# Kernel tuning notes

Measured on AMD Instinct MI355X. Metric: run time of the kernel, lower is better.

Reference implementation:

```python
import jax, jax.numpy as jnp
import numpy as np

# ---- config (matches init_kwargs) ----
M, N, D = 8, 512, 243            # meshes, neurons per mesh, input dim
E_RATIO = 0.8
NE = int(N * E_RATIO)            # 409 excitatory
NI = N - NE                      # 103 inhibitory
TICKS = 16
BATCH = 512
BITS = 4
WSCALE = 8.0
VTH, VRESET = 1.0, 0.0
TAU_E, TAU_I, DT = 2.0, 1.5, 1.0
BETA = 10.0                      # fast-sigmoid surrogate slope
INPUT_SCALE = 1.0


def fake_quant(w):
    """Quantization-aware fake quant with straight-through estimator."""
    step = WSCALE / (2 ** (BITS - 1))          # 1.0 for 4-bit, scale 8
    q = jnp.clip(jnp.round(w / step), -(2 ** (BITS - 1)), 2 ** (BITS - 1) - 1) * step
    return w + jax.lax.stop_gradient(q - w)


@jax.custom_vjp
def spike(u):
    return (u >= 0.0).astype(u.dtype)

def _spike_fwd(u):
    return spike(u), u

def _spike_bwd(u, g):
    # fast-sigmoid surrogate gradient
    return (g * BETA / (1.0 + BETA * jnp.abs(u)) ** 2,)

spike.defvjp(_spike_fwd, _spike_bwd)


def setup_inputs() -> dict:
    key = jax.random.key(0)
    ks = jax.random.split(key, 8)

    def sparse_w(k, shape, density, std, zero_diag=False):
        km, kw = jax.random.split(k)
        mask = (jax.random.uniform(km, shape) < density).astype(jnp.float32)
        if zero_diag:
            mask = mask * (1.0 - jnp.eye(shape[-1], dtype=jnp.float32))
        return jax.random.normal(kw, shape) * std * mask

    x = jax.random.normal(ks[0], (BATCH, D), dtype=jnp.float32)
    W_in = jax.random.normal(ks[1], (M, N, D)) * 0.8      # per-mesh input projection [out,in]
    b_in = jax.random.normal(ks[2], (M, N)) * 0.05
    W_inter = sparse_w(ks[3], (M, N, NE), 0.3, 0.8)        # inter-mesh: E of mesh m -> mesh m+1
    W_EE = sparse_w(ks[4], (M, NE, NE), 0.5, 0.8, True)
    W_EI = sparse_w(ks[5], (M, NI, NE), 0.6, 0.8)
    W_IE = sparse_w(ks[6], (M, NE, NI), 0.8, 0.8)
    W_II = sparse_w(ks[7], (M, NI, NI), 0.7, 0.8, True)
    return dict(x=x, W_in=W_in, b_in=b_in, W_inter=W_inter,
                W_EE=W_EE, W_EI=W_EI, W_IE=W_IE, W_II=W_II)


def reference(x, W_in, b_in, W_inter, W_EE, W_EI, W_IE, W_II):
    B = x.shape[0]
    decay_E = 1.0 - DT / TAU_E
    decay_I = 1.0 - DT / TAU_I

    # quantize weights once (constant across ticks)
    qW_in, qW_inter = fake_quant(W_in), fake_quant(W_inter)
    qW_EE, qW_EI = fake_quant(W_EE), fake_quant(W_EI)
    qW_IE, qW_II = fake_quant(W_IE), fake_quant(W_II)

    # external input projection, same every tick: [M, B, N]
    ext_proj = jnp.einsum('bd,mnd->mbn', x * INPUT_SCALE, qW_in) + b_in[:, None, :]

    def tick(carry, _):
        e, i, vE, vI, acc = carry          # e:[M,B,NE] i:[M,B,NI]
        # inter-mesh: mesh m receives inter_connections[m-1](e_prev[m-1])
        inter = jnp.einsum('mbe,mne->mbn', e, qW_inter)
        ext = ext_proj + jnp.roll(inter, 1, axis=0)
        cE = ext[:, :, :NE] \
            + jnp.einsum('mbe,mfe->mbf', e, qW_EE) \
            + jnp.einsum('mbi,mfi->mbf', i, qW_IE)
        cI = ext[:, :, NE:] \
            + jnp.einsum('mbe,mfe->mbf', e, qW_EI) \
            + jnp.einsum('mbi,mfi->mbf', i, qW_II)
        # LIF: leaky decay + input, threshold, hard reset
        vE = vE * decay_E + cE * DT
        vI = vI * decay_I + cI * DT
        sE = spike(vE - VTH)
        sI = spike(vI - VTH)
        vE = sE * VRESET + (1.0 - sE) * vE
        vI = sI * VRESET + (1.0 - sI) * vI
        acc = acc + jnp.concatenate([sE, sI], axis=-1)
        return (sE, sI, vE, vI, acc), None

    z = jnp.zeros
    carry0 = (z((M, B, NE)), z((M, B, NI)), z((M, B, NE)), z((M, B, NI)), z((M, B, N)))
    (eF, iF, vEF, vIF, acc), _ = jax.lax.scan(tick, carry0, None, length=TICKS)
    # accumulator laid out mesh-major: [B, M*N]
    return jnp.transpose(acc, (1, 0, 2)).reshape(B, M * N)
```

## Files before the change

### kernel.cpp

```cpp
#include <hip/hip_runtime.h>
#include <hip/hip_bf16.h>

#define Mm 8
#define Nn 512
#define NEe 409
#define NIi 103
#define Bb 512
#define Dd 243
#define Tt 16
#define SPB 96
#define SPTICK (Mm * Bb * SPB)
#define WCROW 1152
#define DEC_I 0.33333334f
#define NBLK 256
#define FLAGSTRIDE 16
#define SPINMAX 1000000L
#define ABROW 176
#define ZSPAN_U32 1581056

typedef int v4i __attribute__((ext_vector_type(4)));

__device__ __forceinline__ float quantf(float w) {
    float q = rintf(w);
    return fminf(fmaxf(q, -8.0f), 7.0f);
}

__device__ __forceinline__ v4i unpack16(unsigned int dl, unsigned int dh, bool qhi, int qsh) {
    unsigned int d = qhi ? dh : dl;
    v4i r;
    r[0] = (int)((((d >> qsh) & 0xFu) * 0x00204081u) & 0x01010101u);
    r[1] = (int)((((d >> (qsh + 4)) & 0xFu) * 0x00204081u) & 0x01010101u);
    r[2] = (int)((((d >> (qsh + 8)) & 0xFu) * 0x00204081u) & 0x01010101u);
    r[3] = (int)((((d >> (qsh + 12)) & 0xFu) * 0x00204081u) & 0x01010101u);
    return r;
}

__global__ void k_pack(const float* __restrict__ Wint, const float* __restrict__ WEE,
                       const float* __restrict__ WEI, const float* __restrict__ WIE,
                       const float* __restrict__ WII, signed char* __restrict__ Wc,
                       unsigned* __restrict__ spz) {
    int gid = blockIdx.x * 256 + threadIdx.x;
#pragma unroll
    for (int z = 0; z < 2; ++z) {
        int i = gid + z * 1179648;
        if (i < ZSPAN_U32) spz[i] = 0u;
    }
    int q = gid;
    if (q >= (Mm * Nn * WCROW) / 4) return;
    int k0 = (q * 4) % WCROW;
    int n  = ((q * 4) / WCROW) & (Nn - 1);
    int m  = (q * 4) / (WCROW * Nn);
    char out4[4];
#pragma unroll
    for (int j = 0; j < 4; ++j) {
        int k = k0 + j;
        float w = 0.0f;
        if (k < 512) {
            if (k < NEe) w = Wint[((((m + 7) & 7) * Nn) + n) * NEe + k];
        } else if (k < 1024) {
            int jj = k - 512;
            if (jj < NEe) w = (n < NEe) ? WEE[((m * NEe) + n) * NEe + jj]
                                        : WEI[((m * NIi) + (n - NEe)) * NEe + jj];
        } else {
            int jj = k - 1049;
            if (jj >= 0 && jj < NIi) w = (n < NEe) ? WIE[((m * NEe) + n) * NIi + jj]
                                        : WII[((m * NIi) + (n - NEe)) * NIi + jj];
        }
        out4[j] = (signed char)(int)quantf(w);
    }
    *(int*)&Wc[q * 4] = *(int*)out4;
}

__global__ void __launch_bounds__(512, 2)
k_ticks(const signed char* __restrict__ Wc,
        unsigned char* __restrict__ Sp,
        const float* __restrict__ x,
        const float* __restrict__ Win,
        const float* __restrict__ bin,
        float* __restrict__ out,
        int* __restrict__ flags) {
    __shared__ __align__(16) signed char sB[128 * WCROW];
    __shared__ __align__(16) unsigned char sAb[64 * ABROW];

    const int wg = blockIdx.x;
    const int m  = wg & 7;
    const int bt = (wg >> 3) & 7;
    const int nt = wg >> 6;
    const int b0 = bt * 64;
    const int n0 = nt * 128;
    const int pm = (m + 7) & 7;

    const int tid  = threadIdx.x;
    const int w    = tid >> 6;
    const int lane = tid & 63;
    const int bh   = w & 1;
    const int nh   = w >> 1;
    const int quad = lane >> 4;
    const int li   = lane & 15;

    int waitIdx = 0;
    if (tid < 8) {
        int mm = (tid < 4) ? pm : m;
        waitIdx = (((tid & 3) << 6) | (bt << 3) | mm) * FLAGSTRIDE;
    }

    float decs[2]; int nels[2];
    int styp[2], soff[2];
#pragma unroll
    for (int tn = 0; tn < 2; ++tn) {
        int n = n0 + nh * 32 + tn * 16 + li;
        nels[tn] = n;
        decs[tn] = (n < NEe) ? 0.5f : DEC_I;
        int nb = n0 + nh * 32 + tn * 16;
        if (nb < 400)      { styp[tn] = 0; soff[tn] = nb >> 3; }
        else if (nb == 400){ styp[tn] = 2; soff[tn] = 50; }
        else               { styp[tn] = 1; soff[tn] = 64 + ((nb - 384) >> 3); }
    }
    const int bbase = b0 + bh * 32;

    {
        const int g   = tid >> 8;
        const int t8  = tid & 255;
        const int n0e = n0 + g * 64;
        float* xs  = (float*)sB + g * (2 * 64 * 68);
        float* wsm = xs + 64 * 68;
        const int etb4 = (t8 & 15) * 4;
        const int etn4 = (t8 >> 4) * 4;
        const int sr = t8 >> 2;
        const int sc = (t8 & 3) * 16;
        float c[4][4];
#pragma unroll
        for (int i = 0; i < 4; ++i)
#pragma unroll
            for (int j = 0; j < 4; ++j) c[i][j] = 0.0f;

        for (int d0 = 0; d0 < Dd; d0 += 64) {
#pragma unroll
            for (int j = 0; j < 16; ++j) {
                int d = d0 + sc + j;
                float xv = 0.0f, wv = 0.0f;
                if (d < Dd) {
                    xv = x[(b0 + sr) * Dd + d];
                    wv = quantf(Win[((m * Nn) + n0e + sr) * Dd + d]);
                }
                xs[(sc + j) * 68 + sr] = xv;
                wsm[(sc + j) * 68 + sr] = wv;
            }
            __syncthreads();
            const int dmax = min(64, Dd - d0);
            for (int d = 0; d < dmax; ++d) {
                float4 av = *(const float4*)&xs[d * 68 + etb4];
                float4 wv = *(const float4*)&wsm[d * 68 + etn4];
                float a[4] = {av.x, av.y, av.z, av.w};
                float wq[4] = {wv.x, wv.y, wv.z, wv.w};
#pragma unroll
                for (int i = 0; i < 4; ++i)
#pragma unroll
                    for (int j = 0; j < 4; ++j)
                        c[i][j] = fmaf(a[i], wq[j], c[i][j]);
            }
            __syncthreads();
        }
        float* extbuf = (float*)sB;
#pragma unroll
        for (int i = 0; i < 4; ++i)
#pragma unroll
            for (int j = 0; j < 4; ++j)
                extbuf[(etb4 + i) * 128 + g * 64 + etn4 + j] =
                    __fadd_rn(c[i][j], bin[m * Nn + n0e + etn4 + j]);
        __syncthreads();
    }

    float extr[2][2][4];
#pragma unroll
    for (int tb = 0; tb < 2; ++tb)
#pragma unroll
        for (int tn = 0; tn < 2; ++tn)
#pragma unroll
            for (int r = 0; r < 4; ++r)
                extr[tb][tn][r] = ((const float*)sB)[(bh * 32 + tb * 16 + quad * 4 + r) * 128
                                                     + (nels[tn] - n0)];
    __syncthreads();

    const signed char* WcBase = Wc + (size_t)(m * Nn + n0) * WCROW;
#pragma unroll
    for (int j = 0; j < 18; ++j) {
        int task = tid + j * 512;
        int row = task / 72, gg = task % 72;
        v4i v = *(const v4i*)(WcBase + (size_t)row * WCROW + gg * 16);
        int gs = (gg < 64) ? ((gg & 48) | ((gg ^ row) & 15))
                           : (64 + ((gg ^ row) & 7));
        *(v4i*)&sB[row * WCROW + gs * 16] = v;
    }
    if (tid < 384) {
        int row = tid / 6, z = tid - (tid / 6) * 6;
        int s = (z < 3) ? (13 + z) : (26 + z);
        *(unsigned*)&sAb[row * ABROW + s * 4] = 0u;
    }
    __syncthreads();

    float vmem[2][2][4];
    int cnt[2][2];
#pragma unroll
    for (int tb = 0; tb < 2; ++tb)
#pragma unroll
        for (int tn = 0; tn < 2; ++tn) {
            cnt[tb][tn] = 0;
#pragma unroll
            for (int r = 0; r < 4; ++r) vmem[tb][tn][r] = 0.0f;
        }

    const bool qhi = (quad >= 2);
    const int qsh = (quad & 1) << 4;
    const int r0base = (bh * 32 + li) * ABROW;
    const int r1base = (bh * 32 + 16 + li) * ABROW;

    for (int t = 0; t < Tt; ++t) {
        float c[2][2][4];

        if (t == 0) {
#pragma unroll
            for (int tb = 0; tb < 2; ++tb)
#pragma unroll
                for (int tn = 0; tn < 2; ++tn)
#pragma unroll
                    for (int r = 0; r < 4; ++r)
                        c[tb][tn][r] = __fadd_rn(__fadd_rn(__fadd_rn(extr[tb][tn][r], 0.0f), 0.0f), 0.0f);
        } else {
            if (tid < 8) {
                long spin = 0;
                while (__hip_atomic_load(&flags[waitIdx],
                                         __ATOMIC_RELAXED, __HIP_MEMORY_SCOPE_AGENT) < t) {
                    __builtin_amdgcn_s_sleep(2);
                    if (++spin > SPINMAX) break;
                }
            }
            __syncthreads();

            const unsigned char* SR = Sp + (size_t)(t - 1) * SPTICK;
            const unsigned char* PrevRow = SR + (size_t)(pm * Bb + b0) * SPB;
            const unsigned char* OwnRow  = SR + (size_t)(m  * Bb + b0) * SPB;
#pragma unroll
            for (int j = 0; j < 3; ++j) {
                int task = tid + j * 512;
                if (task < 1152) {
                    int row = task / 18, s = task % 18;
                    const unsigned char* src;
                    int dstoff;
                    if (s < 8)       { src = PrevRow + (size_t)row * SPB + s * 8;            dstoff = s * 8; }
                    else if (s < 16) { src = OwnRow  + (size_t)row * SPB + (s - 8) * 8;      dstoff = s * 8; }
                    else             { src = OwnRow  + (size_t)row * SPB + 64 + (s - 16) * 8; dstoff = 128 + (s - 16) * 8; }
                    unsigned long long vb = __hip_atomic_load((const unsigned long long*)src,
                                               __ATOMIC_RELAXED, __HIP_MEMORY_SCOPE_AGENT);
                    *(unsigned long long*)&sAb[row * ABROW + dstoff] = vb;
                }
            }
            __syncthreads();

            v4i acc[2][2];
#pragma unroll
            for (int tb = 0; tb < 2; ++tb)
#pragma unroll
                for (int tn = 0; tn < 2; ++tn) acc[tb][tn] = (v4i){0, 0, 0, 0};

#pragma unroll
            for (int ch = 0; ch < 4; ++ch) {
                const int cb = ch << 8;
                v4i a0lo = *(const v4i*)&sAb[r0base + (cb >> 3)];
                v4i a0hi = *(const v4i*)&sAb[r0base + (cb >> 3) + 16];
                v4i a1lo = *(const v4i*)&sAb[r1base + (cb >> 3)];
                v4i a1hi = *(const v4i*)&sAb[r1base + (cb >> 3) + 16];
#pragma unroll
                for (int ks = 0; ks < 256; ks += 64) {
                    v4i s0 = (ks < 128) ? a0lo : a0hi;
                    v4i s1 = (ks < 128) ? a1lo : a1hi;
                    const int D0 = ((ks >> 6) & 1) ? 2 : 0;
                    v4i af0 = unpack16((unsigned int)s0[D0], (unsigned int)s0[D0 + 1], qhi, qsh);
                    v4i af1 = unpack16((unsigned int)s1[D0], (unsigned int)s1[D0 + 1], qhi, qsh);
                    const int gs = (cb >> 4) + ((((ks >> 4) + quad) ^ li) & 15);
#pragma unroll
                    for (int tn = 0; tn < 2; ++tn) {
                        const v4i bfr = *(const v4i*)&sB[(nh * 32 + tn * 16 + li) * WCROW + gs * 16];
                        acc[0][tn] = __builtin_amdgcn_mfma_i32_16x16x64_i8(af0, bfr, acc[0][tn], 0, 0, 0);
                        acc[1][tn] = __builtin_amdgcn_mfma_i32_16x16x64_i8(af1, bfr, acc[1][tn], 0, 0, 0);
                    }
                }
                if (ch == 1) {
#pragma unroll
                    for (int tb = 0; tb < 2; ++tb)
#pragma unroll
                        for (int tn = 0; tn < 2; ++tn) {
#pragma unroll
                            for (int r = 0; r < 4; ++r)
                                c[tb][tn][r] = __fadd_rn(extr[tb][tn][r], (float)acc[tb][tn][r]);
                            acc[tb][tn] = (v4i){0, 0, 0, 0};
                        }
                } else if (ch == 3) {
#pragma unroll
                    for (int tb = 0; tb < 2; ++tb)
#pragma unroll
                        for (int tn = 0; tn < 2; ++tn) {
#pragma unroll
                            for (int r = 0; r < 4; ++r)
                                c[tb][tn][r] = __fadd_rn(c[tb][tn][r], (float)acc[tb][tn][r]);
                            acc[tb][tn] = (v4i){0, 0, 0, 0};
                        }
                }
            }
            {
                v4i e0 = *(const v4i*)&sAb[r0base + 128];
                v4i e1 = *(const v4i*)&sAb[r1base + 128];
#pragma unroll
                for (int ks = 0; ks < 128; ks += 64) {
                    const int D0 = (ks >> 6) ? 2 : 0;
                    v4i af0 = unpack16((unsigned int)e0[D0], (unsigned int)e0[D0 + 1], qhi, qsh);
                    v4i af1 = unpack16((unsigned int)e1[D0], (unsigned int)e1[D0 + 1], qhi, qsh);
                    const int gs = 64 + ((((ks >> 4) + quad) ^ li) & 7);
#pragma unroll
                    for (int tn = 0; tn < 2; ++tn) {
                        const v4i bfr = *(const v4i*)&sB[(nh * 32 + tn * 16 + li) * WCROW + gs * 16];
                        acc[0][tn] = __builtin_amdgcn_mfma_i32_16x16x64_i8(af0, bfr, acc[0][tn], 0, 0, 0);
                        acc[1][tn] = __builtin_amdgcn_mfma_i32_16x16x64_i8(af1, bfr, acc[1][tn], 0, 0, 0);
                    }
                }
            }
#pragma unroll
            for (int tb = 0; tb < 2; ++tb)
#pragma unroll
                for (int tn = 0; tn < 2; ++tn)
#pragma unroll
                    for (int r = 0; r < 4; ++r)
                        c[tb][tn][r] = __fadd_rn(c[tb][tn][r], (float)acc[tb][tn][r]);
        }

        int snow[2][2] = {{0, 0}, {0, 0}};
#pragma unroll
        for (int tb = 0; tb < 2; ++tb)
#pragma unroll
            for (int tn = 0; tn < 2; ++tn)
#pragma unroll
                for (int r = 0; r < 4; ++r) {
                    float vn = __fadd_rn(__fmul_rn(vmem[tb][tn][r], decs[tn]), c[tb][tn][r]);
                    int s = (vn >= 1.0f) ? 1 : 0;
                    vmem[tb][tn][r] = s ? 0.0f : vn;
                    cnt[tb][tn] += s << (r * 8);
                    snow[tb][tn] |= s << r;
                }

        if (t < Tt - 1) {
            unsigned char* SW = Sp + (size_t)t * SPTICK;
#pragma unroll
            for (int tb = 0; tb < 2; ++tb)
#pragma unroll
                for (int tn = 0; tn < 2; ++tn)
#pragma unroll
                    for (int r = 0; r < 4; ++r) {
                        unsigned long long mk = __ballot((snow[tb][tn] >> r) & 1);
                        if (li == 0) {
                            unsigned short v = (unsigned short)(mk >> (unsigned)(quad << 4));
                            int row = bbase + tb * 16 + quad * 4 + r;
                            unsigned char* rb = SW + (size_t)(m * Bb + row) * SPB;
                            if (styp[tn] != 2) {
                                __hip_atomic_store((unsigned short*)(rb + soff[tn]), v,
                                                   __ATOMIC_RELAXED, __HIP_MEMORY_SCOPE_AGENT);
                            } else {
                                __hip_atomic_store((unsigned short*)(rb + 50),
                                                   (unsigned short)(v & 0x01FF),
                                                   __ATOMIC_RELAXED, __HIP_MEMORY_SCOPE_AGENT);
                                __hip_atomic_store((unsigned short*)(rb + 66),
                                                   (unsigned short)(v & 0xFE00),
                                                   __ATOMIC_RELAXED, __HIP_MEMORY_SCOPE_AGENT);
                            }
                        }
                    }
            __syncthreads();
            if (tid == 0)
                __hip_atomic_store(&flags[wg * FLAGSTRIDE], t + 1,
                                   __ATOMIC_RELAXED, __HIP_MEMORY_SCOPE_AGENT);
        }
    }

#pragma unroll
    for (int tb = 0; tb < 2; ++tb)
#pragma unroll
        for (int tn = 0; tn < 2; ++tn)
#pragma unroll
            for (int r = 0; r < 4; ++r) {
                int b = bbase + tb * 16 + quad * 4 + r;
                out[(size_t)b * (Mm * Nn) + m * Nn + nels[tn]] =
                    (float)((cnt[tb][tn] >> (r * 8)) & 0xff);
            }
}

extern "C" void kernel_launch(void* const* d_in, const int* in_sizes, int n_in,
                              void* d_out, int out_size, void* d_ws, size_t ws_size,
                              hipStream_t stream) {
    const float* x    = (const float*)d_in[0];
    const float* Win  = (const float*)d_in[1];
    const float* bin  = (const float*)d_in[2];
    const float* Wint = (const float*)d_in[3];
    const float* WEE  = (const float*)d_in[4];
    const float* WEI  = (const float*)d_in[5];
    const float* WIE  = (const float*)d_in[6];
    const float* WII  = (const float*)d_in[7];
    float* out = (float*)d_out;

    char* ws = (char*)d_ws;
    signed char* Wc   = (signed char*)ws;
    unsigned char* Sp = (unsigned char*)(ws + 4718592);
    int* flags = (int*)(ws + 4718592 + 16 * SPTICK);

    k_pack<<<(Mm * Nn * WCROW / 4 + 255) / 256, 256, 0, stream>>>(Wint, WEE, WEI, WIE, WII, Wc,
                                                                  (unsigned*)Sp);
    k_ticks<<<NBLK, 512, 0, stream>>>(Wc, Sp, x, Win, bin, out, flags);
}
```

Baseline: 197.0 us.

## Keep quantized weight fragments in registers instead of LDS across all ticks

Each wave now loads its persistent int8 weight fragments (36 v4i per lane) straight from global memory into registers once, and the MFMA loop reads B operands from those registers instead of from a swizzled shared-memory tile. This removes the 147 KB LDS weight buffer and the per-MFMA LDS reads, shrinking shared memory to a small staging area for the input projection. The cost is about 144 extra VGPRs per lane, which under launch_bounds(512,2) may cause spills or limit occupancy. The global loads are uncoalesced per-lane 16-byte strided reads, but they happen only once.

```diff
diff --git a/kernel.cpp b/kernel.cpp
--- a/kernel.cpp
+++ b/kernel.cpp
@@ -79,7 +79,7 @@
         const float* __restrict__ bin,
         float* __restrict__ out,
         int* __restrict__ flags) {
-    __shared__ __align__(16) signed char sB[128 * WCROW];
+    __shared__ __align__(16) float sExt[2][2][64][68];
     __shared__ __align__(16) unsigned char sAb[64 * ABROW];
 
     const int wg = blockIdx.x;
@@ -122,8 +122,8 @@
         const int g   = tid >> 8;
         const int t8  = tid & 255;
         const int n0e = n0 + g * 64;
-        float* xs  = (float*)sB + g * (2 * 64 * 68);
-        float* wsm = xs + 64 * 68;
+        float* xs  = &sExt[g][0][0][0];
+        float* wsm = &sExt[g][1][0][0];
         const int etb4 = (t8 & 15) * 4;
         const int etn4 = (t8 >> 4) * 4;
         const int sr = t8 >> 2;
@@ -161,7 +161,7 @@
             }
             __syncthreads();
         }
-        float* extbuf = (float*)sB;
+        float* extbuf = (float*)sExt;
 #pragma unroll
         for (int i = 0; i < 4; ++i)
 #pragma unroll
@@ -178,20 +178,23 @@
         for (int tn = 0; tn < 2; ++tn)
 #pragma unroll
             for (int r = 0; r < 4; ++r)
-                extr[tb][tn][r] = ((const float*)sB)[(bh * 32 + tb * 16 + quad * 4 + r) * 128
-                                                     + (nels[tn] - n0)];
-    __syncthreads();
-
-    const signed char* WcBase = Wc + (size_t)(m * Nn + n0) * WCROW;
-#pragma unroll
-    for (int j = 0; j < 18; ++j) {
-        int task = tid + j * 512;
-        int row = task / 72, gg = task % 72;
-        v4i v = *(const v4i*)(WcBase + (size_t)row * WCROW + gg * 16);
-        int gs = (gg < 64) ? ((gg & 48) | ((gg ^ row) & 15))
-                           : (64 + ((gg ^ row) & 7));
-        *(v4i*)&sB[row * WCROW + gs * 16] = v;
-    }
+                extr[tb][tn][r] = ((const float*)sExt)[(bh * 32 + tb * 16 + quad * 4 + r) * 128
+                                                       + (nels[tn] - n0)];
+
+    v4i breg[2][18];
+#pragma unroll
+    for (int tn = 0; tn < 2; ++tn) {
+        const signed char* wr = Wc + (size_t)(m * Nn + n0 + nh * 32 + tn * 16 + li) * WCROW
+                              + quad * 16;
+#pragma unroll
+        for (int ch = 0; ch < 4; ++ch)
+#pragma unroll
+            for (int ki = 0; ki < 4; ++ki)
+                breg[tn][ch * 4 + ki] = *(const v4i*)(wr + ch * 256 + ki * 64);
+        breg[tn][16] = *(const v4i*)(wr + 1024);
+        breg[tn][17] = *(const v4i*)(wr + 1024 + 64);
+    }
+
     if (tid < 384) {
         int row = tid / 6, z = tid - (tid / 6) * 6;
         int s = (z < 3) ? (13 + z) : (26 + z);
@@ -271,18 +274,16 @@
                 v4i a1lo = *(const v4i*)&sAb[r1base + (cb >> 3)];
                 v4i a1hi = *(const v4i*)&sAb[r1base + (cb >> 3) + 16];
 #pragma unroll
-                for (int ks = 0; ks < 256; ks += 64) {
-                    v4i s0 = (ks < 128) ? a0lo : a0hi;
-                    v4i s1 = (ks < 128) ? a1lo : a1hi;
-                    const int D0 = ((ks >> 6) & 1) ? 2 : 0;
+                for (int ki = 0; ki < 4; ++ki) {
+                    v4i s0 = (ki < 2) ? a0lo : a0hi;
+                    v4i s1 = (ki < 2) ? a1lo : a1hi;
+                    const int D0 = (ki & 1) ? 2 : 0;
                     v4i af0 = unpack16((unsigned int)s0[D0], (unsigned int)s0[D0 + 1], qhi, qsh);
                     v4i af1 = unpack16((unsigned int)s1[D0], (unsigned int)s1[D0 + 1], qhi, qsh);
-                    const int gs = (cb >> 4) + ((((ks >> 4) + quad) ^ li) & 15);
 #pragma unroll
                     for (int tn = 0; tn < 2; ++tn) {
-                        const v4i bfr = *(const v4i*)&sB[(nh * 32 + tn * 16 + li) * WCROW + gs * 16];
-                        acc[0][tn] = __builtin_amdgcn_mfma_i32_16x16x64_i8(af0, bfr, acc[0][tn], 0, 0, 0);
-                        acc[1][tn] = __builtin_amdgcn_mfma_i32_16x16x64_i8(af1, bfr, acc[1][tn], 0, 0, 0);
+                        acc[0][tn] = __builtin_amdgcn_mfma_i32_16x16x64_i8(af0, breg[tn][ch * 4 + ki], acc[0][tn], 0, 0, 0);
+                        acc[1][tn] = __builtin_amdgcn_mfma_i32_16x16x64_i8(af1, breg[tn][ch * 4 + ki], acc[1][tn], 0, 0, 0);
                     }
                 }
                 if (ch == 1) {
@@ -311,16 +312,14 @@
                 v4i e0 = *(const v4i*)&sAb[r0base + 128];
                 v4i e1 = *(const v4i*)&sAb[r1base + 128];
 #pragma unroll
-                for (int ks = 0; ks < 128; ks += 64) {
-                    const int D0 = (ks >> 6) ? 2 : 0;
+                for (int ki = 0; ki < 2; ++ki) {
+                    const int D0 = ki ? 2 : 0;
                     v4i af0 = unpack16((unsigned int)e0[D0], (unsigned int)e0[D0 + 1], qhi, qsh);
                     v4i af1 = unpack16((unsigned int)e1[D0], (unsigned int)e1[D0 + 1], qhi, qsh);
-                    const int gs = 64 + ((((ks >> 4) + quad) ^ li) & 7);
 #pragma unroll
                     for (int tn = 0; tn < 2; ++tn) {
-                        const v4i bfr = *(const v4i*)&sB[(nh * 32 + tn * 16 + li) * WCROW + gs * 16];
-                        acc[0][tn] = __builtin_amdgcn_mfma_i32_16x16x64_i8(af0, bfr, acc[0][tn], 0, 0, 0);
-                        acc[1][tn] = __builtin_amdgcn_mfma_i32_16x16x64_i8(af1, bfr, acc[1][tn], 0, 0, 0);
+                        acc[0][tn] = __builtin_amdgcn_mfma_i32_16x16x64_i8(af0, breg[tn][16 + ki], acc[0][tn], 0, 0, 0);
+                        acc[1][tn] = __builtin_amdgcn_mfma_i32_16x16x64_i8(af1, breg[tn][16 + ki], acc[1][tn], 0, 0, 0);
                     }
                 }
             }
```

New measurement: 210.2 us. 6.7% more time.

## Replace block-wide barriers with per-wave flag polling and per-wave spike staging

Applied to the files above, without the earlier changes.

Each wave now polls the inter-block tick flags itself, using a wave-wide vote, instead of eight threads polling and then a __syncthreads. Each wave copies only the 32 spike rows its batch half needs into LDS and waits on its own LDS writes, so both block barriers per tick go away. The aim is to stop fast waves waiting on slow ones at every tick. The cost is that the four waves sharing a batch half each load the same rows, multiplying global traffic. Without a barrier, a wave that runs ahead may overwrite shared LDS rows that a sibling is still reading from the previous tick.

```diff
diff --git a/kernel.cpp b/kernel.cpp
--- a/kernel.cpp
+++ b/kernel.cpp
@@ -98,11 +98,8 @@
     const int quad = lane >> 4;
     const int li   = lane & 15;
 
-    int waitIdx = 0;
-    if (tid < 8) {
-        int mm = (tid < 4) ? pm : m;
-        waitIdx = (((tid & 3) << 6) | (bt << 3) | mm) * FLAGSTRIDE;
-    }
+    const int mmW = (lane < 4) ? pm : m;
+    const int waitIdxW = (((lane & 3) << 6) | (bt << 3) | mmW) * FLAGSTRIDE;
 
     float decs[2]; int nels[2];
     int styp[2], soff[2];
@@ -227,35 +224,39 @@
                     for (int r = 0; r < 4; ++r)
                         c[tb][tn][r] = __fadd_rn(__fadd_rn(__fadd_rn(extr[tb][tn][r], 0.0f), 0.0f), 0.0f);
         } else {
-            if (tid < 8) {
+            {
                 long spin = 0;
-                while (__hip_atomic_load(&flags[waitIdx],
-                                         __ATOMIC_RELAXED, __HIP_MEMORY_SCOPE_AGENT) < t) {
-                    __builtin_amdgcn_s_sleep(2);
+                for (;;) {
+                    int f = 0;
+                    if (lane < 8)
+                        f = __hip_atomic_load(&flags[waitIdxW],
+                                              __ATOMIC_RELAXED, __HIP_MEMORY_SCOPE_AGENT);
+                    if (__all((lane < 8) ? (f >= t) : 1)) break;
+                    __builtin_amdgcn_s_sleep(1);
                     if (++spin > SPINMAX) break;
                 }
             }
-            __syncthreads();
 
             const unsigned char* SR = Sp + (size_t)(t - 1) * SPTICK;
             const unsigned char* PrevRow = SR + (size_t)(pm * Bb + b0) * SPB;
             const unsigned char* OwnRow  = SR + (size_t)(m  * Bb + b0) * SPB;
 #pragma unroll
-            for (int j = 0; j < 3; ++j) {
-                int task = tid + j * 512;
-                if (task < 1152) {
-                    int row = task / 18, s = task % 18;
-                    const unsigned char* src;
-                    int dstoff;
-                    if (s < 8)       { src = PrevRow + (size_t)row * SPB + s * 8;            dstoff = s * 8; }
-                    else if (s < 16) { src = OwnRow  + (size_t)row * SPB + (s - 8) * 8;      dstoff = s * 8; }
-                    else             { src = OwnRow  + (size_t)row * SPB + 64 + (s - 16) * 8; dstoff = 128 + (s - 16) * 8; }
-                    unsigned long long vb = __hip_atomic_load((const unsigned long long*)src,
-                                               __ATOMIC_RELAXED, __HIP_MEMORY_SCOPE_AGENT);
-                    *(unsigned long long*)&sAb[row * ABROW + dstoff] = vb;
-                }
-            }
-            __syncthreads();
+            for (int j = 0; j < 9; ++j) {
+                int task = lane + j * 64;
+                int rl = task / 18;
+                int s  = task - rl * 18;
+                int rr = bh * 32 + rl;
+                const unsigned char* src;
+                int dstoff;
+                if (s < 8)       { src = PrevRow + (size_t)rr * SPB + s * 8;            dstoff = s * 8; }
+                else if (s < 16) { src = OwnRow  + (size_t)rr * SPB + (s - 8) * 8;      dstoff = s * 8; }
+                else             { src = OwnRow  + (size_t)rr * SPB + 64 + (s - 16) * 8; dstoff = 128 + (s - 16) * 8; }
+                unsigned long long vb = __hip_atomic_load((const unsigned long long*)src,
+                                           __ATOMIC_RELAXED, __HIP_MEMORY_SCOPE_AGENT);
+                *(unsigned long long*)&sAb[rr * ABROW + dstoff] = vb;
+            }
+            asm volatile("s_waitcnt lgkmcnt(0)" ::: "memory");
+            __builtin_amdgcn_sched_barrier(0);
 
             v4i acc[2][2];
 #pragma unroll
```

Result: slower. 226.7 us (+15.1%).

## Fuse weight quantize-pack into tick kernel and zero workspace with memset

Applied to the files above, without the earlier changes.

Removes the separate k_pack launch and instead has each tick workgroup read the float weights directly, quantize them, and pack 16 int8 values per thread task into shared memory. The spike/flag workspace zeroing is replaced with hipMemsetAsync. This avoids one kernel launch and the round trip of writing and re-reading the packed int8 weight buffer. In exchange, the persistent kernel's prologue now does scattered, uncoalesced 4-byte float loads with heavy branching, which may lengthen its startup.

```diff
diff --git a/kernel.cpp b/kernel.cpp
--- a/kernel.cpp
+++ b/kernel.cpp
@@ -16,9 +16,9 @@
 #define FLAGSTRIDE 16
 #define SPINMAX 1000000L
 #define ABROW 176
-#define ZSPAN_U32 1581056
 
 typedef int v4i __attribute__((ext_vector_type(4)));
+union BV { signed char b[16]; v4i v; };
 
 __device__ __forceinline__ float quantf(float w) {
     float q = rintf(w);
@@ -35,44 +35,10 @@
     return r;
 }
 
-__global__ void k_pack(const float* __restrict__ Wint, const float* __restrict__ WEE,
-                       const float* __restrict__ WEI, const float* __restrict__ WIE,
-                       const float* __restrict__ WII, signed char* __restrict__ Wc,
-                       unsigned* __restrict__ spz) {
-    int gid = blockIdx.x * 256 + threadIdx.x;
-#pragma unroll
-    for (int z = 0; z < 2; ++z) {
-        int i = gid + z * 1179648;
-        if (i < ZSPAN_U32) spz[i] = 0u;
-    }
-    int q = gid;
-    if (q >= (Mm * Nn * WCROW) / 4) return;
-    int k0 = (q * 4) % WCROW;
-    int n  = ((q * 4) / WCROW) & (Nn - 1);
-    int m  = (q * 4) / (WCROW * Nn);
-    char out4[4];
-#pragma unroll
-    for (int j = 0; j < 4; ++j) {
-        int k = k0 + j;
-        float w = 0.0f;
-        if (k < 512) {
-            if (k < NEe) w = Wint[((((m + 7) & 7) * Nn) + n) * NEe + k];
-        } else if (k < 1024) {
-            int jj = k - 512;
-            if (jj < NEe) w = (n < NEe) ? WEE[((m * NEe) + n) * NEe + jj]
-                                        : WEI[((m * NIi) + (n - NEe)) * NEe + jj];
-        } else {
-            int jj = k - 1049;
-            if (jj >= 0 && jj < NIi) w = (n < NEe) ? WIE[((m * NEe) + n) * NIi + jj]
-                                        : WII[((m * NIi) + (n - NEe)) * NIi + jj];
-        }
-        out4[j] = (signed char)(int)quantf(w);
-    }
-    *(int*)&Wc[q * 4] = *(int*)out4;
-}
-
 __global__ void __launch_bounds__(512, 2)
-k_ticks(const signed char* __restrict__ Wc,
+k_ticks(const float* __restrict__ Wint, const float* __restrict__ WEE,
+        const float* __restrict__ WEI, const float* __restrict__ WIE,
+        const float* __restrict__ WII,
         unsigned char* __restrict__ Sp,
         const float* __restrict__ x,
         const float* __restrict__ Win,
@@ -182,15 +148,32 @@
                                                      + (nels[tn] - n0)];
     __syncthreads();
 
-    const signed char* WcBase = Wc + (size_t)(m * Nn + n0) * WCROW;
 #pragma unroll
     for (int j = 0; j < 18; ++j) {
         int task = tid + j * 512;
         int row = task / 72, gg = task % 72;
-        v4i v = *(const v4i*)(WcBase + (size_t)row * WCROW + gg * 16);
+        int n = n0 + row;
+        BV pk;
+#pragma unroll
+        for (int e = 0; e < 16; ++e) {
+            int k = gg * 16 + e;
+            float wv = 0.0f;
+            if (k < 512) {
+                if (k < NEe) wv = Wint[((pm * Nn) + n) * NEe + k];
+            } else if (k < 1024) {
+                int jj = k - 512;
+                if (jj < NEe) wv = (n < NEe) ? WEE[((m * NEe) + n) * NEe + jj]
+                                             : WEI[((m * NIi) + (n - NEe)) * NEe + jj];
+            } else {
+                int jj = k - 1049;
+                if (jj >= 0 && jj < NIi) wv = (n < NEe) ? WIE[((m * NEe) + n) * NIi + jj]
+                                             : WII[((m * NIi) + (n - NEe)) * NIi + jj];
+            }
+            pk.b[e] = (signed char)(int)quantf(wv);
+        }
         int gs = (gg < 64) ? ((gg & 48) | ((gg ^ row) & 15))
                            : (64 + ((gg ^ row) & 7));
-        *(v4i*)&sB[row * WCROW + gs * 16] = v;
+        *(v4i*)&sB[row * WCROW + gs * 16] = pk.v;
     }
     if (tid < 384) {
         int row = tid / 6, z = tid - (tid / 6) * 6;
@@ -406,11 +389,10 @@
     float* out = (float*)d_out;
 
     char* ws = (char*)d_ws;
-    signed char* Wc   = (signed char*)ws;
-    unsigned char* Sp = (unsigned char*)(ws + 4718592);
-    int* flags = (int*)(ws + 4718592 + 16 * SPTICK);
-
-    k_pack<<<(Mm * Nn * WCROW / 4 + 255) / 256, 256, 0, stream>>>(Wint, WEE, WEI, WIE, WII, Wc,
-                                                                  (unsigned*)Sp);
-    k_ticks<<<NBLK, 512, 0, stream>>>(Wc, Sp, x, Win, bin, out, flags);
+    unsigned char* Sp = (unsigned char*)ws;
+    int* flags = (int*)(ws + 16 * SPTICK);
+
+    hipMemsetAsync(ws, 0, 16 * SPTICK + 32768, stream);
+    k_ticks<<<NBLK, 512, 0, stream>>>(Wint, WEE, WEI, WIE, WII,
+                                      Sp, x, Win, bin, out, flags);
 }
```

After: 283.5 us. 1.44x slower.
